# Performance work log

Hardware: AMD Instinct MI355X
Metric: run time of the kernel (lower is better)

Reference implementation:

```python
import jax, jax.numpy as jnp
import numpy as np

BLOCK_SIZE = 1024
OUTLIER_SIGMA = 3.0
OUT_FEATURES = 11008
IN_FEATURES = 4096
TOKENS = 64


def _quantize_mixed_np(W):
    """Faithful numpy port of quantize_mixed (BLOCK_SIZE divides numel exactly here)."""
    flat = W.astype(np.float32).reshape(-1)
    nb = flat.size // BLOCK_SIZE
    blocks = flat.reshape(nb, BLOCK_SIZE)
    mu = blocks.mean(axis=1, keepdims=True)
    sig = np.maximum(blocks.std(axis=1, ddof=1, keepdims=True), 1e-8)  # torch.std is unbiased
    outlier = np.abs(blocks - mu) > OUTLIER_SIGMA * sig
    abs_max = np.maximum(np.abs(np.where(outlier, 0.0, blocks)).max(axis=1), 1e-8)
    scales = (abs_max / 127.0).astype(np.float16)
    q = np.clip(np.round(blocks / abs_max[:, None] * 127.0), -127, 127).astype(np.int8)
    all_pos = np.arange(nb, dtype=np.int64)[:, None] * BLOCK_SIZE + np.arange(BLOCK_SIZE, dtype=np.int64)[None, :]
    int8_data = q[~outlier]                      # row-major == torch order
    fp16_data = blocks[outlier].astype(np.float16)
    int8_pos = all_pos[~outlier].astype(np.int32)
    fp16_pos = all_pos[outlier].astype(np.int32)
    block_idx = np.nonzero(~outlier)[0].astype(np.int32)  # block index per int8 value
    return int8_data, fp16_data, scales, int8_pos, fp16_pos, block_idx


def setup_inputs() -> dict:
    key = jax.random.key(0)
    k_x, k_b = jax.random.split(key)
    rng = np.random.default_rng(0)
    W = (rng.standard_normal((OUT_FEATURES, IN_FEATURES)) * 0.02).astype(np.float32)
    int8_data, fp16_data, scales, int8_pos, fp16_pos, block_idx = _quantize_mixed_np(W)
    x = jax.random.normal(k_x, (TOKENS, IN_FEATURES), dtype=jnp.float16)
    bias = jax.random.normal(k_b, (OUT_FEATURES,), dtype=jnp.float16) * jnp.float16(0.02)
    return {
        "x": x,
        "int8_data": jnp.asarray(int8_data),
        "fp16_data": jnp.asarray(fp16_data),
        "scales": jnp.asarray(scales),
        "bias": bias,
        "int8_pos": jnp.asarray(int8_pos),
        "fp16_pos": jnp.asarray(fp16_pos),
        "block_idx": jnp.asarray(block_idx),
    }


def reference(x, int8_data, fp16_data, scales, bias, int8_pos, fp16_pos, block_idx):
    out_features = bias.shape[0]
    in_features = x.shape[1]
    numel = out_features * in_features  # divisible by BLOCK_SIZE for these dims
    # dequantize_mixed: scatter fp16 outliers and dequantized int8 values into flat fp16 buffer
    flat = jnp.zeros((numel,), dtype=jnp.float16)
    flat = flat.at[fp16_pos].set(fp16_data)
    flat = flat.at[int8_pos].set(int8_data.astype(jnp.float16) * scales[block_idx])
    W = flat.reshape(out_features, in_features)
    # F.linear(x, W, bias) in fp16
    return jnp.dot(x.astype(jnp.float16), W.T) + bias
```

## Files before the change

kernel.cpp:

```cpp
#include <hip/hip_runtime.h>
#include <hip/hip_fp16.h>

#define TOK   64
#define INF   4096
#define OUTF  11008
#define NUMEL (OUTF * INF)
#define NSLC  (NUMEL / 64)
#define NQB   (NUMEL / 1024)
#define NBLK  (OUTF / 16)
#define KSPL  4

typedef __attribute__((ext_vector_type(8))) _Float16 half8;
typedef __attribute__((ext_vector_type(4))) _Float16 half4;
typedef __attribute__((ext_vector_type(4))) float floatx4;
typedef __attribute__((ext_vector_type(4), aligned(4))) int int4u;

__global__ __launch_bounds__(256) void precompute_kernel(
    const float* __restrict__ x, const int* __restrict__ fppos, int nf,
    _Float16* __restrict__ x16, int* __restrict__ cum64) {
  const int t = blockIdx.x * 256 + threadIdx.x;
  if (t < (TOK * INF) / 4) {
    const floatx4 f = *(const floatx4*)&x[t * 4];
    half4 h;
    h[0] = (_Float16)f[0]; h[1] = (_Float16)f[1];
    h[2] = (_Float16)f[2]; h[3] = (_Float16)f[3];
    *(half4*)&x16[t * 4] = h;
  }
  if (t <= NSLC) {
    const int target = t << 6;
    int lo = 0, hi = nf;
    while (lo < hi) {
      const int mid = (lo + hi) >> 1;
      if (fppos[mid] < target) lo = mid + 1; else hi = mid;
    }
    cum64[t] = lo;
  }
}

__global__ __launch_bounds__(256) void dequant_kernel(
    const int* __restrict__ i8, const float* __restrict__ fpdat,
    const int* __restrict__ fppos, const float* __restrict__ scales,
    const int* __restrict__ cum64, _Float16* __restrict__ W, int n8) {
  const int t   = blockIdx.x * 256 + threadIdx.x;
  const int p0  = t * 8;
  const int s64 = p0 >> 6;
  const int c0  = cum64[s64];
  const int c1  = cum64[s64 + 1];
  const float s = scales[p0 >> 10];

  int lt = 0, f = 0;
  float ov[8];
#pragma unroll
  for (int e = 0; e < 8; ++e) ov[e] = 0.f;

  const int w = c1 - c0;
  if (w > 0) {
    {
      const int d = fppos[c0] - p0;
      const float v = fpdat[c0];
      lt += (d < 0);
      if ((unsigned)d < 8u) {
        f |= 1 << d;
#pragma unroll
        for (int e = 0; e < 8; ++e) ov[e] = (d == e) ? v : ov[e];
      }
    }
    if (w > 1) {
      const int d = fppos[c0 + 1] - p0;
      const float v = fpdat[c0 + 1];
      lt += (d < 0);
      if ((unsigned)d < 8u) {
        f |= 1 << d;
#pragma unroll
        for (int e = 0; e < 8; ++e) ov[e] = (d == e) ? v : ov[e];
      }
    }
    for (int j = 2; j < w; ++j) {
      const int d = fppos[c0 + j] - p0;
      const float v = fpdat[c0 + j];
      lt += (d < 0);
      if ((unsigned)d < 8u) {
        f |= 1 << d;
#pragma unroll
        for (int e = 0; e < 8; ++e) ov[e] = (d == e) ? v : ov[e];
      }
    }
  }

  const int i0 = p0 - c0 - lt;
  half8 oh;
  if (i0 + 8 <= n8) {
    int l[8];
    *(int4u*)&l[0] = *(const int4u*)&i8[i0];
    *(int4u*)&l[4] = *(const int4u*)&i8[i0 + 4];
    if (f == 0) {
#pragma unroll
      for (int e = 0; e < 8; ++e) oh[e] = (_Float16)((float)l[e] * s);
    } else {
      int q = 0;
#pragma unroll
      for (int e = 0; e < 8; ++e) {
        const int flg = (f >> e) & 1;
        int lv = l[0];
#pragma unroll
        for (int qq = 1; qq < 8; ++qq) lv = (q == qq) ? l[qq] : lv;
        oh[e] = flg ? (_Float16)ov[e] : (_Float16)((float)lv * s);
        q += 1 - flg;
      }
    }
  } else {
    int c = 0;
    const int m = n8 - 1;
#pragma unroll
    for (int e = 0; e < 8; ++e) {
      const int flg = (f >> e) & 1;
      int idx = i0 + e - c;
      idx = idx < 0 ? 0 : (idx > m ? m : idx);
      oh[e] = flg ? (_Float16)ov[e] : (_Float16)((float)i8[idx] * s);
      c += flg;
    }
  }
  *(half8*)&W[p0] = oh;
}

__global__ __launch_bounds__(256) void gemm_kernel(
    const _Float16* __restrict__ x16, const _Float16* __restrict__ W,
    const float* __restrict__ bias, float* __restrict__ out) {
  __shared__ float red[4 * 64 * 16];

  const int tid  = threadIdx.x;
  const int wave = tid >> 6;
  const int lane = tid & 63;
  const int quad = lane >> 4;
  const int ln   = lane & 15;
  const int nt   = blockIdx.x >> 2;
  const int kq   = blockIdx.x & 3;
  const int n0   = nt * 16;

  const int kb = kq * 1024 + wave * 256 + quad * 8;
  const _Float16* wp = &W[(n0 + ln) * INF + kb];
  const _Float16* ap = &x16[ln * INF + kb];

  floatx4 acc0 = {0,0,0,0}, acc1 = {0,0,0,0}, acc2 = {0,0,0,0}, acc3 = {0,0,0,0};
#pragma unroll
  for (int st = 0; st < 8; ++st) {
    const int ko = st * 32;
    const half8 bh = *(const half8*)&wp[ko];
    const half8 a0 = *(const half8*)&ap[ko];
    const half8 a1 = *(const half8*)&ap[16 * INF + ko];
    const half8 a2 = *(const half8*)&ap[32 * INF + ko];
    const half8 a3 = *(const half8*)&ap[48 * INF + ko];
    acc0 = __builtin_amdgcn_mfma_f32_16x16x32_f16(a0, bh, acc0, 0, 0, 0);
    acc1 = __builtin_amdgcn_mfma_f32_16x16x32_f16(a1, bh, acc1, 0, 0, 0);
    acc2 = __builtin_amdgcn_mfma_f32_16x16x32_f16(a2, bh, acc2, 0, 0, 0);
    acc3 = __builtin_amdgcn_mfma_f32_16x16x32_f16(a3, bh, acc3, 0, 0, 0);
  }

  const int mb = quad * 4;
#pragma unroll
  for (int i = 0; i < 4; ++i) red[wave * 1024 + (mb + i)      * 16 + ln] = acc0[i];
#pragma unroll
  for (int i = 0; i < 4; ++i) red[wave * 1024 + (16 + mb + i) * 16 + ln] = acc1[i];
#pragma unroll
  for (int i = 0; i < 4; ++i) red[wave * 1024 + (32 + mb + i) * 16 + ln] = acc2[i];
#pragma unroll
  for (int i = 0; i < 4; ++i) red[wave * 1024 + (48 + mb + i) * 16 + ln] = acc3[i];
  __syncthreads();

#pragma unroll
  for (int c2 = 0; c2 < 4; ++c2) {
    const int cell = tid + c2 * 256;
    const int mm = cell >> 4, nn = cell & 15;
    float v = red[cell] + red[1024 + cell] + red[2048 + cell] + red[3072 + cell];
    if (kq == 0) v += bias[n0 + nn];
    atomicAdd(&out[mm * OUTF + n0 + nn], v);
  }
}

extern "C" void kernel_launch(void* const* d_in, const int* in_sizes, int n_in,
                              void* d_out, int out_size, void* d_ws,
                              size_t ws_size, hipStream_t stream) {
  const float* x      = (const float*)d_in[0];
  const int*   i8     = (const int*)d_in[1];
  const float* fpdat  = (const float*)d_in[2];
  const float* scales = (const float*)d_in[3];
  const float* bias   = (const float*)d_in[4];
  const int*   fppos  = (const int*)d_in[6];

  char* wsp = (char*)d_ws;
  _Float16* W     = (_Float16*)wsp;
  _Float16* x16   = (_Float16*)(wsp + (size_t)NUMEL * sizeof(_Float16));
  int*      cum64 = (int*)(wsp + (size_t)NUMEL * sizeof(_Float16)
                               + (size_t)TOK * INF * sizeof(_Float16));
  float*    out   = (float*)d_out;

  const int n8 = in_sizes[1];
  const int nf = in_sizes[2];

  hipMemsetAsync(out, 0, (size_t)out_size * sizeof(float), stream);
  precompute_kernel<<<(NSLC + 256) / 256 + 1, 256, 0, stream>>>(x, fppos, nf,
                                                                x16, cum64);
  dequant_kernel<<<NUMEL / (8 * 256), 256, 0, stream>>>(i8, fpdat, fppos,
                                                        scales, cum64, W, n8);
  gemm_kernel<<<NBLK * KSPL, 256, 0, stream>>>(x16, W, bias, out);
}
```

Baseline: 471.7 us.

## Widen dequant to 16 elements per thread and drop GEMM split-K atomics

Result: no change. 475.0 us (+0.7%).

```diff
diff --git a/kernel.cpp b/kernel.cpp
--- a/kernel.cpp
+++ b/kernel.cpp
@@ -6,9 +6,7 @@
 #define OUTF  11008
 #define NUMEL (OUTF * INF)
 #define NSLC  (NUMEL / 64)
-#define NQB   (NUMEL / 1024)
 #define NBLK  (OUTF / 16)
-#define KSPL  4
 
 typedef __attribute__((ext_vector_type(8))) _Float16 half8;
 typedef __attribute__((ext_vector_type(4))) _Float16 half4;
@@ -42,69 +40,67 @@
     const int* __restrict__ fppos, const float* __restrict__ scales,
     const int* __restrict__ cum64, _Float16* __restrict__ W, int n8) {
   const int t   = blockIdx.x * 256 + threadIdx.x;
-  const int p0  = t * 8;
+  const int p0  = t * 16;
   const int s64 = p0 >> 6;
   const int c0  = cum64[s64];
   const int c1  = cum64[s64 + 1];
   const float s = scales[p0 >> 10];
 
   int lt = 0, f = 0;
-  float ov[8];
-#pragma unroll
-  for (int e = 0; e < 8; ++e) ov[e] = 0.f;
+  float ov[16];
+#pragma unroll
+  for (int e = 0; e < 16; ++e) ov[e] = 0.f;
 
   const int w = c1 - c0;
   if (w > 0) {
-    {
-      const int d = fppos[c0] - p0;
-      const float v = fpdat[c0];
-      lt += (d < 0);
-      if ((unsigned)d < 8u) {
-        f |= 1 << d;
-#pragma unroll
-        for (int e = 0; e < 8; ++e) ov[e] = (d == e) ? v : ov[e];
-      }
-    }
-    if (w > 1) {
-      const int d = fppos[c0 + 1] - p0;
-      const float v = fpdat[c0 + 1];
-      lt += (d < 0);
-      if ((unsigned)d < 8u) {
-        f |= 1 << d;
-#pragma unroll
-        for (int e = 0; e < 8; ++e) ov[e] = (d == e) ? v : ov[e];
+#pragma unroll 2
+    for (int j = 0; j < 2; ++j) {
+      if (j < w) {
+        const int d = fppos[c0 + j] - p0;
+        const float v = fpdat[c0 + j];
+        lt += (d < 0);
+        if ((unsigned)d < 16u) {
+          f |= 1 << d;
+#pragma unroll
+          for (int e = 0; e < 16; ++e) ov[e] = (d == e) ? v : ov[e];
+        }
       }
     }
     for (int j = 2; j < w; ++j) {
       const int d = fppos[c0 + j] - p0;
       const float v = fpdat[c0 + j];
       lt += (d < 0);
-      if ((unsigned)d < 8u) {
+      if ((unsigned)d < 16u) {
         f |= 1 << d;
 #pragma unroll
-        for (int e = 0; e < 8; ++e) ov[e] = (d == e) ? v : ov[e];
+        for (int e = 0; e < 16; ++e) ov[e] = (d == e) ? v : ov[e];
       }
     }
   }
 
   const int i0 = p0 - c0 - lt;
-  half8 oh;
-  if (i0 + 8 <= n8) {
-    int l[8];
-    *(int4u*)&l[0] = *(const int4u*)&i8[i0];
-    *(int4u*)&l[4] = *(const int4u*)&i8[i0 + 4];
+  half8 oh0, oh1;
+  if (i0 + 16 <= n8) {
+    int l[16];
+    *(int4u*)&l[0]  = *(const int4u*)&i8[i0];
+    *(int4u*)&l[4]  = *(const int4u*)&i8[i0 + 4];
+    *(int4u*)&l[8]  = *(const int4u*)&i8[i0 + 8];
+    *(int4u*)&l[12] = *(const int4u*)&i8[i0 + 12];
     if (f == 0) {
 #pragma unroll
-      for (int e = 0; e < 8; ++e) oh[e] = (_Float16)((float)l[e] * s);
+      for (int e = 0; e < 8; ++e) oh0[e] = (_Float16)((float)l[e] * s);
+#pragma unroll
+      for (int e = 0; e < 8; ++e) oh1[e] = (_Float16)((float)l[8 + e] * s);
     } else {
       int q = 0;
 #pragma unroll
-      for (int e = 0; e < 8; ++e) {
+      for (int e = 0; e < 16; ++e) {
         const int flg = (f >> e) & 1;
         int lv = l[0];
 #pragma unroll
-        for (int qq = 1; qq < 8; ++qq) lv = (q == qq) ? l[qq] : lv;
-        oh[e] = flg ? (_Float16)ov[e] : (_Float16)((float)lv * s);
+        for (int qq = 1; qq < 16; ++qq) lv = (q == qq) ? l[qq] : lv;
+        const _Float16 hv = flg ? (_Float16)ov[e] : (_Float16)((float)lv * s);
+        if (e < 8) oh0[e] = hv; else oh1[e - 8] = hv;
         q += 1 - flg;
       }
     }
@@ -112,38 +108,38 @@
     int c = 0;
     const int m = n8 - 1;
 #pragma unroll
-    for (int e = 0; e < 8; ++e) {
+    for (int e = 0; e < 16; ++e) {
       const int flg = (f >> e) & 1;
       int idx = i0 + e - c;
       idx = idx < 0 ? 0 : (idx > m ? m : idx);
-      oh[e] = flg ? (_Float16)ov[e] : (_Float16)((float)i8[idx] * s);
+      const _Float16 hv = flg ? (_Float16)ov[e] : (_Float16)((float)i8[idx] * s);
+      if (e < 8) oh0[e] = hv; else oh1[e - 8] = hv;
       c += flg;
     }
   }
-  *(half8*)&W[p0] = oh;
-}
-
-__global__ __launch_bounds__(256) void gemm_kernel(
+  *(half8*)&W[p0]     = oh0;
+  *(half8*)&W[p0 + 8] = oh1;
+}
+
+__global__ __launch_bounds__(512) void gemm_kernel(
     const _Float16* __restrict__ x16, const _Float16* __restrict__ W,
     const float* __restrict__ bias, float* __restrict__ out) {
-  __shared__ float red[4 * 64 * 16];
+  __shared__ float red[8 * 64 * 16];
 
   const int tid  = threadIdx.x;
   const int wave = tid >> 6;
   const int lane = tid & 63;
   const int quad = lane >> 4;
   const int ln   = lane & 15;
-  const int nt   = blockIdx.x >> 2;
-  const int kq   = blockIdx.x & 3;
-  const int n0   = nt * 16;
-
-  const int kb = kq * 1024 + wave * 256 + quad * 8;
+  const int n0   = blockIdx.x * 16;
+
+  const int kb = wave * 512 + quad * 8;
   const _Float16* wp = &W[(n0 + ln) * INF + kb];
   const _Float16* ap = &x16[ln * INF + kb];
 
   floatx4 acc0 = {0,0,0,0}, acc1 = {0,0,0,0}, acc2 = {0,0,0,0}, acc3 = {0,0,0,0};
-#pragma unroll
-  for (int st = 0; st < 8; ++st) {
+#pragma unroll 4
+  for (int st = 0; st < 16; ++st) {
     const int ko = st * 32;
     const half8 bh = *(const half8*)&wp[ko];
     const half8 a0 = *(const half8*)&ap[ko];
@@ -168,12 +164,13 @@
   __syncthreads();
 
 #pragma unroll
-  for (int c2 = 0; c2 < 4; ++c2) {
-    const int cell = tid + c2 * 256;
+  for (int c2 = 0; c2 < 2; ++c2) {
+    const int cell = tid + c2 * 512;
     const int mm = cell >> 4, nn = cell & 15;
-    float v = red[cell] + red[1024 + cell] + red[2048 + cell] + red[3072 + cell];
-    if (kq == 0) v += bias[n0 + nn];
-    atomicAdd(&out[mm * OUTF + n0 + nn], v);
+    float v = bias[n0 + nn];
+#pragma unroll
+    for (int wv = 0; wv < 8; ++wv) v += red[wv * 1024 + cell];
+    out[mm * OUTF + n0 + nn] = v;
   }
 }
 
@@ -197,10 +194,9 @@
   const int n8 = in_sizes[1];
   const int nf = in_sizes[2];
 
-  hipMemsetAsync(out, 0, (size_t)out_size * sizeof(float), stream);
   precompute_kernel<<<(NSLC + 256) / 256 + 1, 256, 0, stream>>>(x, fppos, nf,
                                                                 x16, cum64);
-  dequant_kernel<<<NUMEL / (8 * 256), 256, 0, stream>>>(i8, fpdat, fppos,
-                                                        scales, cum64, W, n8);
-  gemm_kernel<<<NBLK * KSPL, 256, 0, stream>>>(x16, W, bias, out);
-}
+  dequant_kernel<<<NUMEL / (16 * 256), 256, 0, stream>>>(i8, fpdat, fppos,
+                                                         scales, cum64, W, n8);
+  gemm_kernel<<<NBLK, 512, 0, stream>>>(x16, W, bias, out);
+}
```
